# Optimization experiments

Hardware: AMD Instinct MI355X
Metric: run time of the kernel (lower is better)

Reference implementation:

```python
import jax, jax.numpy as jnp
import numpy as np

N_NODES = 100000
N_EDGES = 1600000


def gcn_conv(x, edge_index, W, b):
    # PyG GCNConv: add self-loops, symmetric degree normalization,
    # linear transform, scatter-sum aggregation, + bias.
    n = x.shape[0]
    loop = jnp.arange(n, dtype=edge_index.dtype)
    src = jnp.concatenate([edge_index[0], loop])
    dst = jnp.concatenate([edge_index[1], loop])
    deg = jnp.zeros((n,), x.dtype).at[dst].add(1.0)
    dinv = jnp.where(deg > 0, deg ** -0.5, 0.0)
    norm = dinv[src] * dinv[dst]            # [E+N]
    h = x @ W                               # [N, out]
    msg = h[src] * norm[:, None]            # gather + scale
    out = jax.ops.segment_sum(msg, dst, num_segments=n)
    return out + b


def setup_inputs() -> dict:
    key = jax.random.key(0)
    k1, k2, k3, k4 = jax.random.split(key, 4)
    d_in, d_lat, d_out = 512, 128, 64
    x = jax.random.normal(k1, (N_NODES, d_in), jnp.float32)
    edge_index = jax.random.randint(k2, (2, N_EDGES), 0, N_NODES, jnp.int64)
    W1 = jax.random.normal(k3, (d_in, d_lat), jnp.float32) * (d_in ** -0.5)
    b1 = jnp.zeros((d_lat,), jnp.float32)
    W2 = jax.random.normal(k4, (d_lat, d_out), jnp.float32) * (d_lat ** -0.5)
    b2 = jnp.zeros((d_out,), jnp.float32)
    return {"x": x, "edge_index": edge_index, "W1": W1, "b1": b1, "W2": W2, "b2": b2}


def reference(x, edge_index, W1, b1, W2, b2):
    h = gcn_conv(x, edge_index, W1, b1)
    h = gcn_conv(h, edge_index, W2, b2)
    return jax.nn.relu(h)
```

## Files before the change

### kernel.cpp

```cpp
#include <hip/hip_runtime.h>
#include <hip/hip_bf16.h>

typedef unsigned short u16;
typedef unsigned int   u32;

#define N_NODES 100000
#define N_EDGES 1600000
#define NQ      (N_EDGES / 4)
#define SLICE   12500
#define BPG     96

__device__ __forceinline__ float bf2f(u16 u) {
    union { u32 i; float f; } c; c.i = ((u32)u) << 16; return c.f;
}
__device__ __forceinline__ u16 f2bf(float f) {
    union { float f; u32 i; } c; c.f = f;
    u32 u = c.i;
    u += 0x7fffu + ((u >> 16) & 1u);
    return (u16)(u >> 16);
}
__device__ __forceinline__ void acc8(uint4 d, float* a) {
    a[0] += bf2f((u16)(d.x & 0xffffu)); a[1] += bf2f((u16)(d.x >> 16));
    a[2] += bf2f((u16)(d.y & 0xffffu)); a[3] += bf2f((u16)(d.y >> 16));
    a[4] += bf2f((u16)(d.z & 0xffffu)); a[5] += bf2f((u16)(d.z >> 16));
    a[6] += bf2f((u16)(d.w & 0xffffu)); a[7] += bf2f((u16)(d.w >> 16));
}

__global__ __launch_bounds__(256) void k_convert(const u32* __restrict__ ei,
                                                 uint4* __restrict__ src4,
                                                 uint4* __restrict__ dst4) {
    __shared__ int sflag;
    if (threadIdx.x == 0) {
        u32 h = ei[1] | ei[3] | ei[5] | ei[7];
        sflag = (h == 0u) ? 1 : 0;
    }
    __syncthreads();
    int q = blockIdx.x * 256 + threadIdx.x;
    if (q >= NQ) return;
    const uint4* e4 = (const uint4*)ei;
    if (sflag) {
        uint4 a = e4[2 * q],          b = e4[2 * q + 1];
        src4[q] = make_uint4(a.x, a.z, b.x, b.z);
        uint4 c = e4[2 * NQ + 2 * q], d = e4[2 * NQ + 2 * q + 1];
        dst4[q] = make_uint4(c.x, c.z, d.x, d.z);
    } else {
        src4[q] = e4[q];
        dst4[q] = e4[NQ + q];
    }
}

__global__ __launch_bounds__(256) void k_degree(const uint4* __restrict__ dst4,
                                                int* __restrict__ deg) {
    const int g = blockIdx.x & 7, bb = blockIdx.x >> 3;
    const int lo = g * SLICE, hi = lo + SLICE;
    for (int q = bb * 256 + threadIdx.x; q < NQ; q += BPG * 256) {
        uint4 d = dst4[q];
        if ((int)d.x >= lo && (int)d.x < hi) atomicAdd(&deg[d.x], 1);
        if ((int)d.y >= lo && (int)d.y < hi) atomicAdd(&deg[d.y], 1);
        if ((int)d.z >= lo && (int)d.z < hi) atomicAdd(&deg[d.z], 1);
        if ((int)d.w >= lo && (int)d.w < hi) atomicAdd(&deg[d.w], 1);
    }
}

__global__ void k_scan_part(const int* __restrict__ deg, int* __restrict__ rowstart,
                            int* __restrict__ bsums) {
    __shared__ int sh[256];
    const int t = threadIdx.x, b = blockIdx.x;
    const int base = b * 2048 + t * 8;
    int v[8]; int s = 0;
#pragma unroll
    for (int i = 0; i < 8; i++) {
        int idx = base + i;
        v[i] = (idx < N_NODES) ? deg[idx] : 0;
        s += v[i];
    }
    sh[t] = s;
    __syncthreads();
    for (int d = 1; d < 256; d <<= 1) {
        int x = (t >= d) ? sh[t - d] : 0;
        __syncthreads();
        sh[t] += x;
        __syncthreads();
    }
    int acc = sh[t] - s;
#pragma unroll
    for (int i = 0; i < 8; i++) {
        int idx = base + i;
        if (idx < N_NODES) rowstart[idx] = acc;
        acc += v[i];
    }
    if (t == 255) bsums[b] = sh[255];
}

__global__ void k_scan_add_dinv(int* __restrict__ rowstart, const int* __restrict__ bsums,
                                const int* __restrict__ deg, float* __restrict__ dinv,
                                int* __restrict__ cursor) {
    __shared__ int soff;
    const int j = blockIdx.x >> 3;
    if (threadIdx.x < 64) {
        int v = ((int)threadIdx.x < j) ? bsums[threadIdx.x] : 0;
        v += __shfl_xor(v, 1);  v += __shfl_xor(v, 2);  v += __shfl_xor(v, 4);
        v += __shfl_xor(v, 8);  v += __shfl_xor(v, 16); v += __shfl_xor(v, 32);
        if (threadIdx.x == 0) soff = v;
    }
    __syncthreads();
    int i = blockIdx.x * blockDim.x + threadIdx.x;
    if (i < N_NODES) {
        int r = rowstart[i] + soff;
        rowstart[i] = r;
        cursor[i] = r;
        dinv[i] = rsqrtf((float)(deg[i] + 1));
    }
    if (i == 0) rowstart[N_NODES] = N_EDGES;
}

__global__ __launch_bounds__(256) void k_fill(const uint4* __restrict__ dst4,
                                              const int* __restrict__ src32,
                                              int* __restrict__ cursor,
                                              int* __restrict__ csr) {
    const int g = blockIdx.x & 7, bb = blockIdx.x >> 3;
    const int lo = g * SLICE, hi = lo + SLICE;
    for (int q = bb * 256 + threadIdx.x; q < NQ; q += BPG * 256) {
        uint4 d = dst4[q];
        if ((int)d.x >= lo && (int)d.x < hi) csr[atomicAdd(&cursor[d.x], 1)] = src32[4 * q];
        if ((int)d.y >= lo && (int)d.y < hi) csr[atomicAdd(&cursor[d.y], 1)] = src32[4 * q + 1];
        if ((int)d.z >= lo && (int)d.z < hi) csr[atomicAdd(&cursor[d.z], 1)] = src32[4 * q + 2];
        if ((int)d.w >= lo && (int)d.w < hi) csr[atomicAdd(&cursor[d.w], 1)] = src32[4 * q + 3];
    }
}

__global__ __launch_bounds__(256) void k_weights(const float* __restrict__ W1,
                                                 const float* __restrict__ W2,
                                                 const float* __restrict__ b1,
                                                 u16* __restrict__ Bt,
                                                 float* __restrict__ c1) {
    int idx = blockIdx.x * 256 + threadIdx.x;
    int l = idx & 63, c = (idx >> 6) & 3, kt = idx >> 8;
    int n = c * 16 + (l & 15);
    int k0 = kt * 32 + (l >> 4) * 8;
    float accs[8];
#pragma unroll
    for (int r = 0; r < 8; r++) accs[r] = 0.f;
    for (int jj = 0; jj < 128; jj++) {
        float w2v = W2[jj * 64 + n];
#pragma unroll
        for (int r = 0; r < 8; r++) accs[r] += W1[(k0 + r) * 128 + jj] * w2v;
    }
    u32 p[4];
#pragma unroll
    for (int j = 0; j < 4; j++)
        p[j] = (u32)f2bf(accs[2 * j]) | ((u32)f2bf(accs[2 * j + 1]) << 16);
    *(uint4*)&Bt[(long)idx * 8] = make_uint4(p[0], p[1], p[2], p[3]);

    if (blockIdx.x == 0 && threadIdx.x < 64) {
        int nn = threadIdx.x;
        float acc = 0.f;
        for (int j = 0; j < 128; j++) acc += b1[j] * W2[j * 64 + nn];
        c1[nn] = acc;
    }
}


__global__ __launch_bounds__(256) void gemm_x(const float* __restrict__ A,
                                              const u16* __restrict__ Bt,
                                              const float* __restrict__ dinv,
                                              u16* __restrict__ C, int M) {
    constexpr int SA = 40;
    __shared__ u16 As[128 * SA];
    typedef __attribute__((ext_vector_type(8))) short v8s;
    typedef __attribute__((ext_vector_type(4))) float v4f;

    const int t = threadIdx.x;
    const int wave = t >> 6, lane = t & 63;
    const int m = lane & 15, quad = lane >> 4;
    const int row0 = blockIdx.x * 128;

    v4f acc[2][4];
#pragma unroll
    for (int i = 0; i < 2; i++)
#pragma unroll
        for (int c = 0; c < 4; c++)
#pragma unroll
            for (int r = 0; r < 4; r++) acc[i][c][r] = 0.0f;

    const int arow = t >> 1, ahalf = t & 1;
    const long aoff = (long)(row0 + arow) * 512;
    const bool arow_ok = (row0 + arow) < M;

    for (int kt = 0; kt < 16; ++kt) {
        const int kk0 = kt * 32 + ahalf * 16;
        float4 f0 = make_float4(0.f, 0.f, 0.f, 0.f), f1 = f0, f2 = f0, f3 = f0;
        if (arow_ok) {
            f0 = *(const float4*)&A[aoff + kk0];
            f1 = *(const float4*)&A[aoff + kk0 + 4];
            f2 = *(const float4*)&A[aoff + kk0 + 8];
            f3 = *(const float4*)&A[aoff + kk0 + 12];
        }
        uint4 w0, w1;
        w0.x = (u32)f2bf(f0.x) | ((u32)f2bf(f0.y) << 16);
        w0.y = (u32)f2bf(f0.z) | ((u32)f2bf(f0.w) << 16);
        w0.z = (u32)f2bf(f1.x) | ((u32)f2bf(f1.y) << 16);
        w0.w = (u32)f2bf(f1.z) | ((u32)f2bf(f1.w) << 16);
        w1.x = (u32)f2bf(f2.x) | ((u32)f2bf(f2.y) << 16);
        w1.y = (u32)f2bf(f2.z) | ((u32)f2bf(f2.w) << 16);
        w1.z = (u32)f2bf(f3.x) | ((u32)f2bf(f3.y) << 16);
        w1.w = (u32)f2bf(f3.z) | ((u32)f2bf(f3.w) << 16);
        *(uint4*)&As[arow * SA + ahalf * 16] = w0;
        *(uint4*)&As[arow * SA + ahalf * 16 + 8] = w1;
        __syncthreads();
        v8s a0 = *(const v8s*)&As[(wave * 32 + m) * SA + quad * 8];
        v8s a1 = *(const v8s*)&As[(wave * 32 + 16 + m) * SA + quad * 8];
#pragma unroll
        for (int c = 0; c < 4; c++) {
            v8s b = *(const v8s*)&Bt[(long)((kt * 4 + c) * 64 + lane) * 8];
            acc[0][c] = __builtin_amdgcn_mfma_f32_16x16x32_bf16(a0, b, acc[0][c], 0, 0, 0);
            acc[1][c] = __builtin_amdgcn_mfma_f32_16x16x32_bf16(a1, b, acc[1][c], 0, 0, 0);
        }
        __syncthreads();
    }
#pragma unroll
    for (int i = 0; i < 2; i++)
#pragma unroll
        for (int r = 0; r < 4; r++) {
            int grow = row0 + wave * 32 + i * 16 + quad * 4 + r;
            if (grow < M) {
                float w = dinv[grow];
#pragma unroll
                for (int c = 0; c < 4; c++)
                    C[(long)grow * 64 + c * 16 + m] = f2bf(acc[i][c][r] * w);
            }
        }
}


__global__ __launch_bounds__(256) void agg_a(const u16* __restrict__ zp,
                                             const float* __restrict__ dinv,
                                             const int* __restrict__ rowstart,
                                             const int* __restrict__ csr,
                                             u16* __restrict__ yp,
                                             float* __restrict__ sfac) {
    const int wave = threadIdx.x >> 6, lane = threadIdx.x & 63;
    const int n = blockIdx.x * 4 + wave;
    const int g = lane >> 3, l = lane & 7;
    const uint4* z4 = (const uint4*)zp;
    float a[8] = {0.f, 0.f, 0.f, 0.f, 0.f, 0.f, 0.f, 0.f};
    float sd = 0.f;
    const float w0 = dinv[n];
    if (g == 0) {
        acc8(z4[(long)n * 8 + l], a);
        sd = w0;
    }
    const int i1 = rowstart[n + 1];
    int i = rowstart[n] + g;
    for (; i + 8 < i1; i += 16) {
        int s0 = csr[i], s1 = csr[i + 8];
        uint4 d0 = z4[(long)s0 * 8 + l];
        uint4 d1 = z4[(long)s1 * 8 + l];
        sd += dinv[s0] + dinv[s1];
        acc8(d0, a); acc8(d1, a);
    }
    for (; i < i1; i += 8) {
        int s = csr[i];
        uint4 d = z4[(long)s * 8 + l];
        sd += dinv[s];
        acc8(d, a);
    }
#pragma unroll
    for (int j = 0; j < 8; j++) {
        a[j] += __shfl_xor(a[j], 8);
        a[j] += __shfl_xor(a[j], 16);
        a[j] += __shfl_xor(a[j], 32);
    }
    sd += __shfl_xor(sd, 8); sd += __shfl_xor(sd, 16); sd += __shfl_xor(sd, 32);
    if (g == 0) {
        float w2 = w0 * w0;
        uint4 o;
        o.x = (u32)f2bf(a[0] * w2) | ((u32)f2bf(a[1] * w2) << 16);
        o.y = (u32)f2bf(a[2] * w2) | ((u32)f2bf(a[3] * w2) << 16);
        o.z = (u32)f2bf(a[4] * w2) | ((u32)f2bf(a[5] * w2) << 16);
        o.w = (u32)f2bf(a[6] * w2) | ((u32)f2bf(a[7] * w2) << 16);
        ((uint4*)yp)[(long)n * 8 + l] = o;
        if (l == 0) sfac[n] = w0 * sd;
    }
}


__global__ __launch_bounds__(256) void agg_b(const u16* __restrict__ yp,
                                             const float* __restrict__ dinv,
                                             const int* __restrict__ rowstart,
                                             const int* __restrict__ csr,
                                             const float* __restrict__ sfac,
                                             const float* __restrict__ c1,
                                             const float* __restrict__ b2,
                                             float* __restrict__ out) {
    const int wave = threadIdx.x >> 6, lane = threadIdx.x & 63;
    const int n = blockIdx.x * 4 + wave;
    const int g = lane >> 3, l = lane & 7;
    const uint4* y4 = (const uint4*)yp;
    float a[8] = {0.f, 0.f, 0.f, 0.f, 0.f, 0.f, 0.f, 0.f};
    if (g == 0) acc8(y4[(long)n * 8 + l], a);
    const int i1 = rowstart[n + 1];
    int i = rowstart[n] + g;
    for (; i + 8 < i1; i += 16) {
        int s0 = csr[i], s1 = csr[i + 8];
        uint4 d0 = y4[(long)s0 * 8 + l];
        uint4 d1 = y4[(long)s1 * 8 + l];
        acc8(d0, a); acc8(d1, a);
    }
    for (; i < i1; i += 8) {
        uint4 d = y4[(long)csr[i] * 8 + l];
        acc8(d, a);
    }
#pragma unroll
    for (int j = 0; j < 8; j++) {
        a[j] += __shfl_xor(a[j], 8);
        a[j] += __shfl_xor(a[j], 16);
        a[j] += __shfl_xor(a[j], 32);
    }
    if (g == 0) {
        const float w0 = dinv[n];
        const float sn = sfac[n];
        float4 c0 = ((const float4*)c1)[2 * l], c4 = ((const float4*)c1)[2 * l + 1];
        float4 b0 = ((const float4*)b2)[2 * l], b4 = ((const float4*)b2)[2 * l + 1];
        float4 r0, r1;
        r0.x = fmaxf(a[0] * w0 + sn * c0.x + b0.x, 0.f);
        r0.y = fmaxf(a[1] * w0 + sn * c0.y + b0.y, 0.f);
        r0.z = fmaxf(a[2] * w0 + sn * c0.z + b0.z, 0.f);
        r0.w = fmaxf(a[3] * w0 + sn * c0.w + b0.w, 0.f);
        r1.x = fmaxf(a[4] * w0 + sn * c4.x + b4.x, 0.f);
        r1.y = fmaxf(a[5] * w0 + sn * c4.y + b4.y, 0.f);
        r1.z = fmaxf(a[6] * w0 + sn * c4.z + b4.z, 0.f);
        r1.w = fmaxf(a[7] * w0 + sn * c4.w + b4.w, 0.f);
        ((float4*)out)[(long)n * 16 + 2 * l]     = r0;
        ((float4*)out)[(long)n * 16 + 2 * l + 1] = r1;
    }
}


extern "C" void kernel_launch(void* const* d_in, const int* in_sizes, int n_in,
                              void* d_out, int out_size, void* d_ws, size_t ws_size,
                              hipStream_t stream) {
    const float* x  = (const float*)d_in[0];
    const u32*   ei = (const u32*)d_in[1];
    const float* W1 = (const float*)d_in[2];
    const float* b1 = (const float*)d_in[3];
    const float* W2 = (const float*)d_in[4];
    const float* b2 = (const float*)d_in[5];
    float* out = (float*)d_out;

    char* ws = (char*)d_ws;
    size_t o = 0;
    auto alloc = [&](size_t bytes) -> char* {
        char* p = ws + o;
        o = (o + bytes + 255) & ~(size_t)255;
        return p;
    };
    int*   deg      = (int*)  alloc(N_NODES * 4);
    float* dinv     = (float*)alloc(N_NODES * 4);
    int*   rowstart = (int*)  alloc((N_NODES + 1) * 4);
    int*   cursor   = (int*)  alloc(N_NODES * 4);
    int*   bsums    = (int*)  alloc(64 * 4);
    u16*   Bt       = (u16*)  alloc(512 * 64 * 2);
    float* c1       = (float*)alloc(64 * 4);
    float* sfac     = (float*)alloc(N_NODES * 4);
    uint4* src4     = (uint4*)alloc((size_t)N_EDGES * 4);
    uint4* dst4     = (uint4*)alloc((size_t)N_EDGES * 4);
    int*   csr      = (int*)  alloc((size_t)N_EDGES * 4);
    u16*   z        = (u16*)  alloc((size_t)N_NODES * 64 * 2);
    u16*   y        = (u16*)  alloc((size_t)N_NODES * 64 * 2);
    (void)ws_size;

    hipMemsetAsync(deg, 0, N_NODES * 4, stream);

    const int NB = (N_NODES + 255) / 256;
    const int CQ = (NQ + 255) / 256;

    k_convert<<<CQ, 256, 0, stream>>>(ei, src4, dst4);
    k_degree<<<8 * BPG, 256, 0, stream>>>(dst4, deg);
    k_scan_part<<<(N_NODES + 2047) / 2048, 256, 0, stream>>>(deg, rowstart, bsums);
    k_scan_add_dinv<<<NB, 256, 0, stream>>>(rowstart, bsums, deg, dinv, cursor);
    k_fill<<<8 * BPG, 256, 0, stream>>>(dst4, (const int*)src4, cursor, csr);

    k_weights<<<16, 256, 0, stream>>>(W1, W2, b1, Bt, c1);

    gemm_x<<<(N_NODES + 127) / 128, 256, 0, stream>>>(x, Bt, dinv, z, N_NODES);
    agg_a<<<N_NODES / 4, 256, 0, stream>>>(z, dinv, rowstart, csr, y, sfac);
    agg_b<<<N_NODES / 4, 256, 0, stream>>>(y, dinv, rowstart, csr, sfac, c1, b2, out);
}
```

Measured before the change: 578.1 us.

## Fuse both aggregation passes into one persistent kernel with a grid barrier

Merges agg_a and agg_b into a single persistent kernel of 1024 blocks that grid-strides over node quads. An atomic counter plus a spin flag acts as a grid-wide barrier between the two aggregation phases. This removes one kernel launch and its drain/ramp gap. In exchange it caps occupancy at 1024 blocks, adds a spin-wait whose progress depends on every block being co-resident, and ties the second phase to the slowest block of the first.

```diff
diff --git a/kernel.cpp b/kernel.cpp
--- a/kernel.cpp
+++ b/kernel.cpp
@@ -9,6 +9,9 @@
 #define NQ      (N_EDGES / 4)
 #define SLICE   12500
 #define BPG     96
+
+#define NQUADS     (N_NODES / 4)
+#define AGG_BLOCKS 1024
 
 __device__ __forceinline__ float bf2f(u16 u) {
     union { u32 i; float f; } c; c.i = ((u32)u) << 16; return c.f;
@@ -233,106 +236,115 @@
 }
 
 
-__global__ __launch_bounds__(256) void agg_a(const u16* __restrict__ zp,
-                                             const float* __restrict__ dinv,
-                                             const int* __restrict__ rowstart,
-                                             const int* __restrict__ csr,
-                                             u16* __restrict__ yp,
-                                             float* __restrict__ sfac) {
+__global__ __launch_bounds__(256, 4) void agg_fused(const u16* __restrict__ zp,
+                                                    const float* __restrict__ dinv,
+                                                    const int* __restrict__ rowstart,
+                                                    const int* __restrict__ csr,
+                                                    u16* __restrict__ yp,
+                                                    float* __restrict__ sfac,
+                                                    const float* __restrict__ c1,
+                                                    const float* __restrict__ b2,
+                                                    float* __restrict__ out,
+                                                    int* bar) {
     const int wave = threadIdx.x >> 6, lane = threadIdx.x & 63;
-    const int n = blockIdx.x * 4 + wave;
     const int g = lane >> 3, l = lane & 7;
     const uint4* z4 = (const uint4*)zp;
-    float a[8] = {0.f, 0.f, 0.f, 0.f, 0.f, 0.f, 0.f, 0.f};
-    float sd = 0.f;
-    const float w0 = dinv[n];
-    if (g == 0) {
-        acc8(z4[(long)n * 8 + l], a);
-        sd = w0;
-    }
-    const int i1 = rowstart[n + 1];
-    int i = rowstart[n] + g;
-    for (; i + 8 < i1; i += 16) {
-        int s0 = csr[i], s1 = csr[i + 8];
-        uint4 d0 = z4[(long)s0 * 8 + l];
-        uint4 d1 = z4[(long)s1 * 8 + l];
-        sd += dinv[s0] + dinv[s1];
-        acc8(d0, a); acc8(d1, a);
-    }
-    for (; i < i1; i += 8) {
-        int s = csr[i];
-        uint4 d = z4[(long)s * 8 + l];
-        sd += dinv[s];
-        acc8(d, a);
-    }
-#pragma unroll
-    for (int j = 0; j < 8; j++) {
-        a[j] += __shfl_xor(a[j], 8);
-        a[j] += __shfl_xor(a[j], 16);
-        a[j] += __shfl_xor(a[j], 32);
-    }
-    sd += __shfl_xor(sd, 8); sd += __shfl_xor(sd, 16); sd += __shfl_xor(sd, 32);
-    if (g == 0) {
-        float w2 = w0 * w0;
-        uint4 o;
-        o.x = (u32)f2bf(a[0] * w2) | ((u32)f2bf(a[1] * w2) << 16);
-        o.y = (u32)f2bf(a[2] * w2) | ((u32)f2bf(a[3] * w2) << 16);
-        o.z = (u32)f2bf(a[4] * w2) | ((u32)f2bf(a[5] * w2) << 16);
-        o.w = (u32)f2bf(a[6] * w2) | ((u32)f2bf(a[7] * w2) << 16);
-        ((uint4*)yp)[(long)n * 8 + l] = o;
-        if (l == 0) sfac[n] = w0 * sd;
-    }
-}
-
-
-__global__ __launch_bounds__(256) void agg_b(const u16* __restrict__ yp,
-                                             const float* __restrict__ dinv,
-                                             const int* __restrict__ rowstart,
-                                             const int* __restrict__ csr,
-                                             const float* __restrict__ sfac,
-                                             const float* __restrict__ c1,
-                                             const float* __restrict__ b2,
-                                             float* __restrict__ out) {
-    const int wave = threadIdx.x >> 6, lane = threadIdx.x & 63;
-    const int n = blockIdx.x * 4 + wave;
-    const int g = lane >> 3, l = lane & 7;
     const uint4* y4 = (const uint4*)yp;
-    float a[8] = {0.f, 0.f, 0.f, 0.f, 0.f, 0.f, 0.f, 0.f};
-    if (g == 0) acc8(y4[(long)n * 8 + l], a);
-    const int i1 = rowstart[n + 1];
-    int i = rowstart[n] + g;
-    for (; i + 8 < i1; i += 16) {
-        int s0 = csr[i], s1 = csr[i + 8];
-        uint4 d0 = y4[(long)s0 * 8 + l];
-        uint4 d1 = y4[(long)s1 * 8 + l];
-        acc8(d0, a); acc8(d1, a);
-    }
-    for (; i < i1; i += 8) {
-        uint4 d = y4[(long)csr[i] * 8 + l];
-        acc8(d, a);
-    }
-#pragma unroll
-    for (int j = 0; j < 8; j++) {
-        a[j] += __shfl_xor(a[j], 8);
-        a[j] += __shfl_xor(a[j], 16);
-        a[j] += __shfl_xor(a[j], 32);
-    }
-    if (g == 0) {
+
+    for (int q = blockIdx.x; q < NQUADS; q += AGG_BLOCKS) {
+        const int n = q * 4 + wave;
+        float a[8] = {0.f, 0.f, 0.f, 0.f, 0.f, 0.f, 0.f, 0.f};
+        float sd = 0.f;
         const float w0 = dinv[n];
-        const float sn = sfac[n];
-        float4 c0 = ((const float4*)c1)[2 * l], c4 = ((const float4*)c1)[2 * l + 1];
-        float4 b0 = ((const float4*)b2)[2 * l], b4 = ((const float4*)b2)[2 * l + 1];
-        float4 r0, r1;
-        r0.x = fmaxf(a[0] * w0 + sn * c0.x + b0.x, 0.f);
-        r0.y = fmaxf(a[1] * w0 + sn * c0.y + b0.y, 0.f);
-        r0.z = fmaxf(a[2] * w0 + sn * c0.z + b0.z, 0.f);
-        r0.w = fmaxf(a[3] * w0 + sn * c0.w + b0.w, 0.f);
-        r1.x = fmaxf(a[4] * w0 + sn * c4.x + b4.x, 0.f);
-        r1.y = fmaxf(a[5] * w0 + sn * c4.y + b4.y, 0.f);
-        r1.z = fmaxf(a[6] * w0 + sn * c4.z + b4.z, 0.f);
-        r1.w = fmaxf(a[7] * w0 + sn * c4.w + b4.w, 0.f);
-        ((float4*)out)[(long)n * 16 + 2 * l]     = r0;
-        ((float4*)out)[(long)n * 16 + 2 * l + 1] = r1;
+        if (g == 0) {
+            acc8(z4[(long)n * 8 + l], a);
+            sd = w0;
+        }
+        const int i1 = rowstart[n + 1];
+        int i = rowstart[n] + g;
+        for (; i + 8 < i1; i += 16) {
+            int s0 = csr[i], s1 = csr[i + 8];
+            uint4 d0 = z4[(long)s0 * 8 + l];
+            uint4 d1 = z4[(long)s1 * 8 + l];
+            sd += dinv[s0] + dinv[s1];
+            acc8(d0, a); acc8(d1, a);
+        }
+        for (; i < i1; i += 8) {
+            int s = csr[i];
+            uint4 d = z4[(long)s * 8 + l];
+            sd += dinv[s];
+            acc8(d, a);
+        }
+#pragma unroll
+        for (int j = 0; j < 8; j++) {
+            a[j] += __shfl_xor(a[j], 8);
+            a[j] += __shfl_xor(a[j], 16);
+            a[j] += __shfl_xor(a[j], 32);
+        }
+        sd += __shfl_xor(sd, 8); sd += __shfl_xor(sd, 16); sd += __shfl_xor(sd, 32);
+        if (g == 0) {
+            float w2 = w0 * w0;
+            uint4 o;
+            o.x = (u32)f2bf(a[0] * w2) | ((u32)f2bf(a[1] * w2) << 16);
+            o.y = (u32)f2bf(a[2] * w2) | ((u32)f2bf(a[3] * w2) << 16);
+            o.z = (u32)f2bf(a[4] * w2) | ((u32)f2bf(a[5] * w2) << 16);
+            o.w = (u32)f2bf(a[6] * w2) | ((u32)f2bf(a[7] * w2) << 16);
+            ((uint4*)yp)[(long)n * 8 + l] = o;
+            if (l == 0) sfac[n] = w0 * sd;
+        }
+    }
+
+    __syncthreads();
+    if (threadIdx.x == 0) {
+        int old = __hip_atomic_fetch_add(&bar[0], 1, __ATOMIC_ACQ_REL, __HIP_MEMORY_SCOPE_AGENT);
+        if (old == AGG_BLOCKS - 1) {
+            __hip_atomic_store(&bar[16], 1, __ATOMIC_RELEASE, __HIP_MEMORY_SCOPE_AGENT);
+        } else {
+            while (__hip_atomic_load(&bar[16], __ATOMIC_ACQUIRE, __HIP_MEMORY_SCOPE_AGENT) == 0)
+                __builtin_amdgcn_s_sleep(2);
+        }
+    }
+    __syncthreads();
+
+    for (int q = blockIdx.x; q < NQUADS; q += AGG_BLOCKS) {
+        const int n = q * 4 + wave;
+        float a[8] = {0.f, 0.f, 0.f, 0.f, 0.f, 0.f, 0.f, 0.f};
+        if (g == 0) acc8(y4[(long)n * 8 + l], a);
+        const int i1 = rowstart[n + 1];
+        int i = rowstart[n] + g;
+        for (; i + 8 < i1; i += 16) {
+            int s0 = csr[i], s1 = csr[i + 8];
+            uint4 d0 = y4[(long)s0 * 8 + l];
+            uint4 d1 = y4[(long)s1 * 8 + l];
+            acc8(d0, a); acc8(d1, a);
+        }
+        for (; i < i1; i += 8) {
+            uint4 d = y4[(long)csr[i] * 8 + l];
+            acc8(d, a);
+        }
+#pragma unroll
+        for (int j = 0; j < 8; j++) {
+            a[j] += __shfl_xor(a[j], 8);
+            a[j] += __shfl_xor(a[j], 16);
+            a[j] += __shfl_xor(a[j], 32);
+        }
+        if (g == 0) {
+            const float w0 = dinv[n];
+            const float sn = sfac[n];
+            float4 c0 = ((const float4*)c1)[2 * l], c4 = ((const float4*)c1)[2 * l + 1];
+            float4 b0 = ((const float4*)b2)[2 * l], b4 = ((const float4*)b2)[2 * l + 1];
+            float4 r0, r1;
+            r0.x = fmaxf(a[0] * w0 + sn * c0.x + b0.x, 0.f);
+            r0.y = fmaxf(a[1] * w0 + sn * c0.y + b0.y, 0.f);
+            r0.z = fmaxf(a[2] * w0 + sn * c0.z + b0.z, 0.f);
+            r0.w = fmaxf(a[3] * w0 + sn * c0.w + b0.w, 0.f);
+            r1.x = fmaxf(a[4] * w0 + sn * c4.x + b4.x, 0.f);
+            r1.y = fmaxf(a[5] * w0 + sn * c4.y + b4.y, 0.f);
+            r1.z = fmaxf(a[6] * w0 + sn * c4.z + b4.z, 0.f);
+            r1.w = fmaxf(a[7] * w0 + sn * c4.w + b4.w, 0.f);
+            ((float4*)out)[(long)n * 16 + 2 * l]     = r0;
+            ((float4*)out)[(long)n * 16 + 2 * l + 1] = r1;
+        }
     }
 }
 
@@ -360,6 +372,7 @@
     int*   rowstart = (int*)  alloc((N_NODES + 1) * 4);
     int*   cursor   = (int*)  alloc(N_NODES * 4);
     int*   bsums    = (int*)  alloc(64 * 4);
+    int*   bar      = (int*)  alloc(256);
     u16*   Bt       = (u16*)  alloc(512 * 64 * 2);
     float* c1       = (float*)alloc(64 * 4);
     float* sfac     = (float*)alloc(N_NODES * 4);
@@ -371,6 +384,7 @@
     (void)ws_size;
 
     hipMemsetAsync(deg, 0, N_NODES * 4, stream);
+    hipMemsetAsync(bar, 0, 256, stream);
 
     const int NB = (N_NODES + 255) / 256;
     const int CQ = (NQ + 255) / 256;
@@ -384,6 +398,5 @@
     k_weights<<<16, 256, 0, stream>>>(W1, W2, b1, Bt, c1);
 
     gemm_x<<<(N_NODES + 127) / 128, 256, 0, stream>>>(x, Bt, dinv, z, N_NODES);
-    agg_a<<<N_NODES / 4, 256, 0, stream>>>(z, dinv, rowstart, csr, y, sfac);
-    agg_b<<<N_NODES / 4, 256, 0, stream>>>(y, dinv, rowstart, csr, sfac, c1, b2, out);
-}
+    agg_fused<<<AGG_BLOCKS, 256, 0, stream>>>(z, dinv, rowstart, csr, y, sfac, c1, b2, out, bar);
+}
```

Result: slower. 796.1 us (+37.7%).

## Aggregate edges per 50-node slice with LDS atomics instead of wave-per-node

Applied to the files above, without the earlier changes.

The CSR now stores (src,dst) pairs, and both aggregation kernels give each block a contiguous slice of 50 destination nodes. Edges are spread evenly across the block's threads and accumulated into padded LDS rows with shared-memory float atomics, then combined with the self-loop term in an epilogue. This is meant to remove the load imbalance and idle lanes of one wave per node, where eight lane groups each walk a short variable-length edge list and then do a shuffle reduction. It costs double the CSR bytes, many LDS atomics with possible contention on popular nodes, and a fill kernel that writes 8-byte entries.

```diff
diff --git a/kernel.cpp b/kernel.cpp
--- a/kernel.cpp
+++ b/kernel.cpp
@@ -10,6 +10,10 @@
 #define SLICE   12500
 #define BPG     96
 
+#define NS      50
+#define NSLICES (N_NODES / NS)
+#define LDW     65
+
 __device__ __forceinline__ float bf2f(u16 u) {
     union { u32 i; float f; } c; c.i = ((u32)u) << 16; return c.f;
 }
@@ -19,11 +23,11 @@
     u += 0x7fffu + ((u >> 16) & 1u);
     return (u16)(u >> 16);
 }
-__device__ __forceinline__ void acc8(uint4 d, float* a) {
-    a[0] += bf2f((u16)(d.x & 0xffffu)); a[1] += bf2f((u16)(d.x >> 16));
-    a[2] += bf2f((u16)(d.y & 0xffffu)); a[3] += bf2f((u16)(d.y >> 16));
-    a[4] += bf2f((u16)(d.z & 0xffffu)); a[5] += bf2f((u16)(d.z >> 16));
-    a[6] += bf2f((u16)(d.w & 0xffffu)); a[7] += bf2f((u16)(d.w >> 16));
+__device__ __forceinline__ void up8(uint4 d, float* f) {
+    f[0] = bf2f((u16)(d.x & 0xffffu)); f[1] = bf2f((u16)(d.x >> 16));
+    f[2] = bf2f((u16)(d.y & 0xffffu)); f[3] = bf2f((u16)(d.y >> 16));
+    f[4] = bf2f((u16)(d.z & 0xffffu)); f[5] = bf2f((u16)(d.z >> 16));
+    f[6] = bf2f((u16)(d.w & 0xffffu)); f[7] = bf2f((u16)(d.w >> 16));
 }
 
 __global__ __launch_bounds__(256) void k_convert(const u32* __restrict__ ei,
@@ -117,15 +121,19 @@
 __global__ __launch_bounds__(256) void k_fill(const uint4* __restrict__ dst4,
                                               const int* __restrict__ src32,
                                               int* __restrict__ cursor,
-                                              int* __restrict__ csr) {
+                                              int2* __restrict__ csr2) {
     const int g = blockIdx.x & 7, bb = blockIdx.x >> 3;
     const int lo = g * SLICE, hi = lo + SLICE;
     for (int q = bb * 256 + threadIdx.x; q < NQ; q += BPG * 256) {
         uint4 d = dst4[q];
-        if ((int)d.x >= lo && (int)d.x < hi) csr[atomicAdd(&cursor[d.x], 1)] = src32[4 * q];
-        if ((int)d.y >= lo && (int)d.y < hi) csr[atomicAdd(&cursor[d.y], 1)] = src32[4 * q + 1];
-        if ((int)d.z >= lo && (int)d.z < hi) csr[atomicAdd(&cursor[d.z], 1)] = src32[4 * q + 2];
-        if ((int)d.w >= lo && (int)d.w < hi) csr[atomicAdd(&cursor[d.w], 1)] = src32[4 * q + 3];
+        if ((int)d.x >= lo && (int)d.x < hi)
+            csr2[atomicAdd(&cursor[d.x], 1)] = make_int2(src32[4 * q],     (int)d.x);
+        if ((int)d.y >= lo && (int)d.y < hi)
+            csr2[atomicAdd(&cursor[d.y], 1)] = make_int2(src32[4 * q + 1], (int)d.y);
+        if ((int)d.z >= lo && (int)d.z < hi)
+            csr2[atomicAdd(&cursor[d.z], 1)] = make_int2(src32[4 * q + 2], (int)d.z);
+        if ((int)d.w >= lo && (int)d.w < hi)
+            csr2[atomicAdd(&cursor[d.w], 1)] = make_int2(src32[4 * q + 3], (int)d.w);
     }
 }
 
@@ -236,51 +244,60 @@
 __global__ __launch_bounds__(256) void agg_a(const u16* __restrict__ zp,
                                              const float* __restrict__ dinv,
                                              const int* __restrict__ rowstart,
-                                             const int* __restrict__ csr,
+                                             const int2* __restrict__ csr2,
                                              u16* __restrict__ yp,
                                              float* __restrict__ sfac) {
-    const int wave = threadIdx.x >> 6, lane = threadIdx.x & 63;
-    const int n = blockIdx.x * 4 + wave;
-    const int g = lane >> 3, l = lane & 7;
+    __shared__ float acc[NS * LDW];
+    __shared__ float sdl[NS];
+    const int tid = threadIdx.x;
+    for (int i = tid; i < NS * LDW; i += 256) acc[i] = 0.f;
+    if (tid < NS) sdl[tid] = 0.f;
+    __syncthreads();
+
+    const int n0 = blockIdx.x * NS;
+    const int e0 = rowstart[n0], e1 = rowstart[n0 + NS];
+    const int r = tid & 7, slot = tid >> 3;
     const uint4* z4 = (const uint4*)zp;
-    float a[8] = {0.f, 0.f, 0.f, 0.f, 0.f, 0.f, 0.f, 0.f};
-    float sd = 0.f;
-    const float w0 = dinv[n];
-    if (g == 0) {
-        acc8(z4[(long)n * 8 + l], a);
-        sd = w0;
-    }
-    const int i1 = rowstart[n + 1];
-    int i = rowstart[n] + g;
-    for (; i + 8 < i1; i += 16) {
-        int s0 = csr[i], s1 = csr[i + 8];
-        uint4 d0 = z4[(long)s0 * 8 + l];
-        uint4 d1 = z4[(long)s1 * 8 + l];
-        sd += dinv[s0] + dinv[s1];
-        acc8(d0, a); acc8(d1, a);
-    }
-    for (; i < i1; i += 8) {
-        int s = csr[i];
-        uint4 d = z4[(long)s * 8 + l];
-        sd += dinv[s];
-        acc8(d, a);
-    }
-#pragma unroll
-    for (int j = 0; j < 8; j++) {
-        a[j] += __shfl_xor(a[j], 8);
-        a[j] += __shfl_xor(a[j], 16);
-        a[j] += __shfl_xor(a[j], 32);
-    }
-    sd += __shfl_xor(sd, 8); sd += __shfl_xor(sd, 16); sd += __shfl_xor(sd, 32);
-    if (g == 0) {
-        float w2 = w0 * w0;
+
+    for (int e = e0 + slot; e < e1; e += 64) {
+        const int e2 = e + 32;
+        const bool h2 = e2 < e1;
+        int2 ed0 = csr2[e];
+        int2 ed1;
+        if (h2) ed1 = csr2[e2];
+        uint4 d0 = z4[(long)ed0.x * 8 + r];
+        uint4 d1;
+        if (h2) d1 = z4[(long)ed1.x * 8 + r];
+        float f[8];
+        up8(d0, f);
+        float* row = &acc[(ed0.y - n0) * LDW + r * 8];
+#pragma unroll
+        for (int j = 0; j < 8; j++) atomicAdd(&row[j], f[j]);
+        if (r == 0) atomicAdd(&sdl[ed0.y - n0], dinv[ed0.x]);
+        if (h2) {
+            up8(d1, f);
+            float* row1 = &acc[(ed1.y - n0) * LDW + r * 8];
+#pragma unroll
+            for (int j = 0; j < 8; j++) atomicAdd(&row1[j], f[j]);
+            if (r == 0) atomicAdd(&sdl[ed1.y - n0], dinv[ed1.x]);
+        }
+    }
+    __syncthreads();
+
+    for (int nn = slot; nn < NS; nn += 32) {
+        const int n = n0 + nn;
+        const float w0 = dinv[n];
+        const float w2 = w0 * w0;
+        float f[8];
+        up8(z4[(long)n * 8 + r], f);
+        const float* row = &acc[nn * LDW + r * 8];
         uint4 o;
-        o.x = (u32)f2bf(a[0] * w2) | ((u32)f2bf(a[1] * w2) << 16);
-        o.y = (u32)f2bf(a[2] * w2) | ((u32)f2bf(a[3] * w2) << 16);
-        o.z = (u32)f2bf(a[4] * w2) | ((u32)f2bf(a[5] * w2) << 16);
-        o.w = (u32)f2bf(a[6] * w2) | ((u32)f2bf(a[7] * w2) << 16);
-        ((uint4*)yp)[(long)n * 8 + l] = o;
-        if (l == 0) sfac[n] = w0 * sd;
+        o.x = (u32)f2bf((f[0] + row[0]) * w2) | ((u32)f2bf((f[1] + row[1]) * w2) << 16);
+        o.y = (u32)f2bf((f[2] + row[2]) * w2) | ((u32)f2bf((f[3] + row[3]) * w2) << 16);
+        o.z = (u32)f2bf((f[4] + row[4]) * w2) | ((u32)f2bf((f[5] + row[5]) * w2) << 16);
+        o.w = (u32)f2bf((f[6] + row[6]) * w2) | ((u32)f2bf((f[7] + row[7]) * w2) << 16);
+        ((uint4*)yp)[(long)n * 8 + r] = o;
+        if (r == 0) sfac[n] = w0 * (w0 + sdl[nn]);
     }
 }
 
@@ -288,51 +305,64 @@
 __global__ __launch_bounds__(256) void agg_b(const u16* __restrict__ yp,
                                              const float* __restrict__ dinv,
                                              const int* __restrict__ rowstart,
-                                             const int* __restrict__ csr,
+                                             const int2* __restrict__ csr2,
                                              const float* __restrict__ sfac,
                                              const float* __restrict__ c1,
                                              const float* __restrict__ b2,
                                              float* __restrict__ out) {
-    const int wave = threadIdx.x >> 6, lane = threadIdx.x & 63;
-    const int n = blockIdx.x * 4 + wave;
-    const int g = lane >> 3, l = lane & 7;
+    __shared__ float acc[NS * LDW];
+    const int tid = threadIdx.x;
+    for (int i = tid; i < NS * LDW; i += 256) acc[i] = 0.f;
+    __syncthreads();
+
+    const int n0 = blockIdx.x * NS;
+    const int e0 = rowstart[n0], e1 = rowstart[n0 + NS];
+    const int r = tid & 7, slot = tid >> 3;
     const uint4* y4 = (const uint4*)yp;
-    float a[8] = {0.f, 0.f, 0.f, 0.f, 0.f, 0.f, 0.f, 0.f};
-    if (g == 0) acc8(y4[(long)n * 8 + l], a);
-    const int i1 = rowstart[n + 1];
-    int i = rowstart[n] + g;
-    for (; i + 8 < i1; i += 16) {
-        int s0 = csr[i], s1 = csr[i + 8];
-        uint4 d0 = y4[(long)s0 * 8 + l];
-        uint4 d1 = y4[(long)s1 * 8 + l];
-        acc8(d0, a); acc8(d1, a);
-    }
-    for (; i < i1; i += 8) {
-        uint4 d = y4[(long)csr[i] * 8 + l];
-        acc8(d, a);
-    }
-#pragma unroll
-    for (int j = 0; j < 8; j++) {
-        a[j] += __shfl_xor(a[j], 8);
-        a[j] += __shfl_xor(a[j], 16);
-        a[j] += __shfl_xor(a[j], 32);
-    }
-    if (g == 0) {
+
+    for (int e = e0 + slot; e < e1; e += 64) {
+        const int e2 = e + 32;
+        const bool h2 = e2 < e1;
+        int2 ed0 = csr2[e];
+        int2 ed1;
+        if (h2) ed1 = csr2[e2];
+        uint4 d0 = y4[(long)ed0.x * 8 + r];
+        uint4 d1;
+        if (h2) d1 = y4[(long)ed1.x * 8 + r];
+        float f[8];
+        up8(d0, f);
+        float* row = &acc[(ed0.y - n0) * LDW + r * 8];
+#pragma unroll
+        for (int j = 0; j < 8; j++) atomicAdd(&row[j], f[j]);
+        if (h2) {
+            up8(d1, f);
+            float* row1 = &acc[(ed1.y - n0) * LDW + r * 8];
+#pragma unroll
+            for (int j = 0; j < 8; j++) atomicAdd(&row1[j], f[j]);
+        }
+    }
+    __syncthreads();
+
+    for (int nn = slot; nn < NS; nn += 32) {
+        const int n = n0 + nn;
         const float w0 = dinv[n];
         const float sn = sfac[n];
-        float4 c0 = ((const float4*)c1)[2 * l], c4 = ((const float4*)c1)[2 * l + 1];
-        float4 b0 = ((const float4*)b2)[2 * l], b4 = ((const float4*)b2)[2 * l + 1];
+        float f[8];
+        up8(y4[(long)n * 8 + r], f);
+        const float* row = &acc[nn * LDW + r * 8];
+        float4 cA = ((const float4*)c1)[r * 2], cB = ((const float4*)c1)[r * 2 + 1];
+        float4 bA = ((const float4*)b2)[r * 2], bB = ((const float4*)b2)[r * 2 + 1];
         float4 r0, r1;
-        r0.x = fmaxf(a[0] * w0 + sn * c0.x + b0.x, 0.f);
-        r0.y = fmaxf(a[1] * w0 + sn * c0.y + b0.y, 0.f);
-        r0.z = fmaxf(a[2] * w0 + sn * c0.z + b0.z, 0.f);
-        r0.w = fmaxf(a[3] * w0 + sn * c0.w + b0.w, 0.f);
-        r1.x = fmaxf(a[4] * w0 + sn * c4.x + b4.x, 0.f);
-        r1.y = fmaxf(a[5] * w0 + sn * c4.y + b4.y, 0.f);
-        r1.z = fmaxf(a[6] * w0 + sn * c4.z + b4.z, 0.f);
-        r1.w = fmaxf(a[7] * w0 + sn * c4.w + b4.w, 0.f);
-        ((float4*)out)[(long)n * 16 + 2 * l]     = r0;
-        ((float4*)out)[(long)n * 16 + 2 * l + 1] = r1;
+        r0.x = fmaxf((f[0] + row[0]) * w0 + sn * cA.x + bA.x, 0.f);
+        r0.y = fmaxf((f[1] + row[1]) * w0 + sn * cA.y + bA.y, 0.f);
+        r0.z = fmaxf((f[2] + row[2]) * w0 + sn * cA.z + bA.z, 0.f);
+        r0.w = fmaxf((f[3] + row[3]) * w0 + sn * cA.w + bA.w, 0.f);
+        r1.x = fmaxf((f[4] + row[4]) * w0 + sn * cB.x + bB.x, 0.f);
+        r1.y = fmaxf((f[5] + row[5]) * w0 + sn * cB.y + bB.y, 0.f);
+        r1.z = fmaxf((f[6] + row[6]) * w0 + sn * cB.z + bB.z, 0.f);
+        r1.w = fmaxf((f[7] + row[7]) * w0 + sn * cB.w + bB.w, 0.f);
+        ((float4*)out)[(long)n * 16 + r * 2]     = r0;
+        ((float4*)out)[(long)n * 16 + r * 2 + 1] = r1;
     }
 }
 
@@ -365,7 +395,7 @@
     float* sfac     = (float*)alloc(N_NODES * 4);
     uint4* src4     = (uint4*)alloc((size_t)N_EDGES * 4);
     uint4* dst4     = (uint4*)alloc((size_t)N_EDGES * 4);
-    int*   csr      = (int*)  alloc((size_t)N_EDGES * 4);
+    int2*  csr2     = (int2*) alloc((size_t)N_EDGES * 8);
     u16*   z        = (u16*)  alloc((size_t)N_NODES * 64 * 2);
     u16*   y        = (u16*)  alloc((size_t)N_NODES * 64 * 2);
     (void)ws_size;
@@ -379,11 +409,11 @@
     k_degree<<<8 * BPG, 256, 0, stream>>>(dst4, deg);
     k_scan_part<<<(N_NODES + 2047) / 2048, 256, 0, stream>>>(deg, rowstart, bsums);
     k_scan_add_dinv<<<NB, 256, 0, stream>>>(rowstart, bsums, deg, dinv, cursor);
-    k_fill<<<8 * BPG, 256, 0, stream>>>(dst4, (const int*)src4, cursor, csr);
+    k_fill<<<8 * BPG, 256, 0, stream>>>(dst4, (const int*)src4, cursor, csr2);
 
     k_weights<<<16, 256, 0, stream>>>(W1, W2, b1, Bt, c1);
 
     gemm_x<<<(N_NODES + 127) / 128, 256, 0, stream>>>(x, Bt, dinv, z, N_NODES);
-    agg_a<<<N_NODES / 4, 256, 0, stream>>>(z, dinv, rowstart, csr, y, sfac);
-    agg_b<<<N_NODES / 4, 256, 0, stream>>>(y, dinv, rowstart, csr, sfac, c1, b2, out);
-}
+    agg_a<<<NSLICES, 256, 0, stream>>>(z, dinv, rowstart, csr2, y, sfac);
+    agg_b<<<NSLICES, 256, 0, stream>>>(y, dinv, rowstart, csr2, sfac, c1, b2, out);
+}
```

After: 1.577 ms. 2.73x slower.
